# Performance work log

Hardware: AMD Instinct MI355X
Metric: run time of the kernel (lower is better)

The kernel has to match this reference:

```python
import jax, jax.numpy as jnp
import numpy as np

NUM_HEADS = 8
NUM_EXPERTS = 16384
NUM_KEYS = 128          # sqrt(NUM_EXPERTS)
TOPK = 16               # num_experts_per_head == product_key_topk
N_DIM = 1024
KEY_DIM = N_DIM // 2


def setup_inputs() -> dict:
    key = jax.random.key(0)
    k1, k2, k3, k4, k5 = jax.random.split(key, 5)
    x = jax.random.normal(k1, (1, 1024, N_DIM), dtype=jnp.float32)
    # torch Linear weight is (out_features, in_features)
    Wq = jax.random.normal(k2, (KEY_DIM * NUM_HEADS * 2, N_DIM), dtype=jnp.float32) * 0.02
    keys = jax.random.normal(k3, (NUM_HEADS, NUM_KEYS, 2, KEY_DIM), dtype=jnp.float32) * 0.02
    up_embed = jax.random.normal(k4, (NUM_EXPERTS * NUM_HEADS, N_DIM), dtype=jnp.float32)
    down_embed = jax.random.normal(k5, (NUM_EXPERTS * NUM_HEADS, N_DIM), dtype=jnp.float32)
    return {"x": x, "Wq": Wq, "keys": keys, "up_embed": up_embed, "down_embed": down_embed}


def reference(x, Wq, keys, up_embed, down_embed):
    b, n, d = x.shape
    # queries: Linear -> (b,n,2,h,kd) -> permute to (2,b,n,h,kd)
    q = (x @ Wq.T).reshape(b, n, 2, NUM_HEADS, KEY_DIM)
    q = jnp.transpose(q, (2, 0, 1, 3, 4))  # (p=2, b, n, h, kd)
    # sim: (p, b, n, h, num_keys)
    sim = jnp.einsum('pbnhd,hkpd->pbnhk', q, keys)
    scores_x, indices_x = jax.lax.top_k(sim[0], TOPK)  # (b,n,h,K)
    scores_y, indices_y = jax.lax.top_k(sim[1], TOPK)
    # cartesian product of the two top-k sets: (b,n,h,K*K)
    all_scores = (scores_x[..., :, None] + scores_y[..., None, :]).reshape(b, n, NUM_HEADS, TOPK * TOPK)
    all_indices = (indices_x[..., :, None] * NUM_KEYS + indices_y[..., None, :]).reshape(b, n, NUM_HEADS, TOPK * TOPK)
    scores, pk_indices = jax.lax.top_k(all_scores, TOPK)  # (b,n,h,K)
    indices = jnp.take_along_axis(all_indices, pk_indices, axis=-1)
    # separate embedding table per head
    head_offsets = jnp.arange(NUM_HEADS, dtype=indices.dtype) * NUM_EXPERTS
    indices = indices + head_offsets[None, None, :, None]
    weights_down = down_embed[indices]  # (b,n,h,K,d)
    weights_up = up_embed[indices]      # (b,n,h,K,d)
    h = jnp.einsum('bnd,bnhkd->bnhk', x, weights_down)
    h = jax.nn.gelu(h, approximate=False)
    h = jax.nn.softmax(scores, axis=-1) * h
    out = jnp.einsum('bnhk,bnhkd->bnd', h, weights_up)
    return out
```

## Files before the change

kernel.cpp:

```cpp
#include <hip/hip_runtime.h>
#include <math.h>


#define BK 16

__device__ __forceinline__ void mac16(double (&acc)[4][4], float4 av, float4 bv) {
  const double ax = av.x, ay = av.y, az = av.z, aw = av.w;
  const double bx = bv.x, by = bv.y, bz = bv.z, bw = bv.w;
  acc[0][0] += ax * bx; acc[0][1] += ax * by; acc[0][2] += ax * bz; acc[0][3] += ax * bw;
  acc[1][0] += ay * bx; acc[1][1] += ay * by; acc[1][2] += ay * bz; acc[1][3] += ay * bw;
  acc[2][0] += az * bx; acc[2][1] += az * by; acc[2][2] += az * bz; acc[2][3] += az * bw;
  acc[3][0] += aw * bx; acc[3][1] += aw * by; acc[3][2] += aw * bz; acc[3][3] += aw * bw;
}

__global__ __launch_bounds__(256) void fold_kernel(
    const float* __restrict__ keys, const float* __restrict__ Wq,
    float* __restrict__ M) {
  __shared__ float As[BK][68];
  __shared__ float Bs[BK][68];
  const int s = blockIdx.z, p = s >> 3, h = s & 7;
  const float* A = keys + h * 131072 + p * 512;
  const float* B = Wq + (p * 4096 + h * 512) * 1024;
  float* C = M + (p * 1024 + h * 128) * 1024;
  const int row0 = blockIdx.y * 64;
  const int d0 = blockIdx.x * 64;
  const int t = threadIdx.x;
  const int tx = t & 15, ty = t >> 4;
  const int arow = t >> 2, ac4 = (t & 3) * 4;
  const int brow = t >> 4, bd4 = (t & 15) * 4;
  double acc[4][4] = {};
  for (int k0 = 0; k0 < 512; k0 += BK) {
    float4 a4 = *(const float4*)(A + (row0 + arow) * 1024 + k0 + ac4);
    float4 b4 = *(const float4*)(B + (k0 + brow) * 1024 + d0 + bd4);
    As[ac4 + 0][arow] = a4.x; As[ac4 + 1][arow] = a4.y;
    As[ac4 + 2][arow] = a4.z; As[ac4 + 3][arow] = a4.w;
    *(float4*)&Bs[brow][bd4] = b4;
    __syncthreads();
#pragma unroll
    for (int kk = 0; kk < BK; ++kk) {
      float4 av = *(const float4*)&As[kk][ty * 4];
      float4 bv = *(const float4*)&Bs[kk][tx * 4];
      mac16(acc, av, bv);
    }
    __syncthreads();
  }
#pragma unroll
  for (int i = 0; i < 4; ++i) {
    float4 o = {(float)acc[i][0], (float)acc[i][1], (float)acc[i][2], (float)acc[i][3]};
    *(float4*)(C + (row0 + ty * 4 + i) * 1024 + d0 + tx * 4) = o;
  }
}

__global__ __launch_bounds__(256) void sim_kernel(
    const float* __restrict__ x, const float* __restrict__ M,
    float* __restrict__ sim) {
  __shared__ float As[BK][68];
  __shared__ float Bs[BK][68];
  const int n0 = blockIdx.y * 64;
  const int r0 = blockIdx.x * 64;
  const int t = threadIdx.x;
  const int tx = t & 15, ty = t >> 4;
  const int arow = t >> 2, ak4 = (t & 3) * 4;
  double acc[4][4] = {};
  for (int k0 = 0; k0 < 1024; k0 += BK) {
    float4 a4 = *(const float4*)(x + (n0 + arow) * 1024 + k0 + ak4);
    float4 b4 = *(const float4*)(M + (r0 + arow) * 1024 + k0 + ak4);
    As[ak4 + 0][arow] = a4.x; As[ak4 + 1][arow] = a4.y;
    As[ak4 + 2][arow] = a4.z; As[ak4 + 3][arow] = a4.w;
    Bs[ak4 + 0][arow] = b4.x; Bs[ak4 + 1][arow] = b4.y;
    Bs[ak4 + 2][arow] = b4.z; Bs[ak4 + 3][arow] = b4.w;
    __syncthreads();
#pragma unroll
    for (int kk = 0; kk < BK; ++kk) {
      float4 av = *(const float4*)&As[kk][ty * 4];
      float4 bv = *(const float4*)&Bs[kk][tx * 4];
      mac16(acc, av, bv);
    }
    __syncthreads();
  }
#pragma unroll
  for (int i = 0; i < 4; ++i) {
    float4 o = {(float)acc[i][0], (float)acc[i][1], (float)acc[i][2], (float)acc[i][3]};
    *(float4*)(sim + (n0 + ty * 4 + i) * 2048 + r0 + tx * 4) = o;
  }
}

__device__ __forceinline__ void insert16(float (&v)[16], int (&id)[16],
                                         float nv, int nid) {
  if (nv > v[15]) {
    v[15] = nv; id[15] = nid;
#pragma unroll
    for (int j = 15; j > 0; --j) {
      if (v[j] > v[j - 1]) {
        float tv = v[j]; v[j] = v[j - 1]; v[j - 1] = tv;
        int ti = id[j]; id[j] = id[j - 1]; id[j - 1] = ti;
      }
    }
  }
}

__global__ __launch_bounds__(256) void topk_kernel(
    const float* __restrict__ sim, int* __restrict__ rows,
    float* __restrict__ wts) {
  const int tid = blockIdx.x * 256 + threadIdx.x;
  const int n = tid >> 3, h = tid & 7;
  const float* sx = sim + n * 2048 + h * 128;
  const float* sy = sx + 1024;
  float vx[16], vy[16]; int ix[16], iy[16];
#pragma unroll
  for (int j = 0; j < 16; ++j) { vx[j] = -1e30f; vy[j] = -1e30f; ix[j] = 0; iy[j] = 0; }
  for (int k = 0; k < 128; ++k) {
    insert16(vx, ix, sx[k], k);
    insert16(vy, iy, sy[k], k);
  }
  constexpr int JMAX[16] = {16, 8, 5, 4, 3, 2, 2, 2, 1, 1, 1, 1, 1, 1, 1, 1};
  float cv[16]; int cid[16];
#pragma unroll
  for (int j = 0; j < 16; ++j) { cv[j] = -1e30f; cid[j] = 0; }
#pragma unroll
  for (int i = 0; i < 16; ++i) {
#pragma unroll
    for (int j = 0; j < 16; ++j) {
      if (j < JMAX[i]) {
        insert16(cv, cid, vx[i] + vy[j], ix[i] * 128 + iy[j]);
      }
    }
  }
  float e[16], se = 0.f;
#pragma unroll
  for (int j = 0; j < 16; ++j) { e[j] = expf(cv[j] - cv[0]); se += e[j]; }
  const float inv = 1.0f / se;
#pragma unroll
  for (int j = 0; j < 16; ++j) {
    rows[tid * 16 + j] = h * 16384 + cid[j];
    wts[tid * 16 + j] = e[j] * inv;
  }
}

__global__ __launch_bounds__(256) void gather_kernel(
    const float* __restrict__ x, const float* __restrict__ up,
    const float* __restrict__ down, const int* __restrict__ rows,
    const float* __restrict__ wts, float* __restrict__ out) {
  __shared__ float xs[1024];
  __shared__ float gs[128];
  __shared__ int rS[128];
  __shared__ float wS[128];
  const int n = blockIdx.x;
  const int t = threadIdx.x;
  ((float4*)xs)[t] = ((const float4*)(x + n * 1024))[t];
  if (t < 128) { rS[t] = rows[n * 128 + t]; wS[t] = wts[n * 128 + t]; }
  __syncthreads();
  const int wave = t >> 6, lane = t & 63;
  const float4* xp = (const float4*)xs;
  for (int it = 0; it < 32; ++it) {
    const int i = it * 4 + wave;
    const long row = rS[i];
    const float4* dp = (const float4*)(down + row * 1024);
    float acc = 0.f;
#pragma unroll
    for (int j = 0; j < 4; ++j) {
      float4 d4 = dp[lane + 64 * j];
      float4 x4 = xp[lane + 64 * j];
      acc += d4.x * x4.x + d4.y * x4.y + d4.z * x4.z + d4.w * x4.w;
    }
#pragma unroll
    for (int off = 32; off; off >>= 1) acc += __shfl_down(acc, off);
    if (lane == 0) {
      const float v = acc;
      const float g = 0.5f * v * (1.0f + erff(v * 0.70710678118654752f));
      gs[i] = g * wS[i];
    }
  }
  __syncthreads();
  float4 a = {0.f, 0.f, 0.f, 0.f};
  const float4* upb = (const float4*)up;
#pragma unroll 4
  for (int i = 0; i < 128; ++i) {
    const long row = rS[i];
    const float g = gs[i];
    float4 u = upb[row * 256 + t];
    a.x += g * u.x; a.y += g * u.y; a.z += g * u.z; a.w += g * u.w;
  }
  ((float4*)out)[n * 256 + t] = a;
}

extern "C" void kernel_launch(void* const* d_in, const int* in_sizes, int n_in,
                              void* d_out, int out_size, void* d_ws, size_t ws_size,
                              hipStream_t stream) {
  const float* x = (const float*)d_in[0];
  const float* Wq = (const float*)d_in[1];
  const float* keys = (const float*)d_in[2];
  const float* up = (const float*)d_in[3];
  const float* down = (const float*)d_in[4];
  float* out = (float*)d_out;
  float* ws = (float*)d_ws;
  float* M = ws;
  float* sim = ws + 2097152;
  int* rows = (int*)(ws + 4194304);
  float* wts = ws + 4325376;

  fold_kernel<<<dim3(16, 2, 16), 256, 0, stream>>>(keys, Wq, M);
  sim_kernel<<<dim3(32, 16, 1), 256, 0, stream>>>(x, M, sim);
  topk_kernel<<<32, 256, 0, stream>>>(sim, rows, wts);
  gather_kernel<<<1024, 256, 0, stream>>>(x, up, down, rows, wts, out);
}
```

Baseline: 1.316 ms.

## Store folded matrix in double, vectorize top-k loads, batch gather rows

```diff
diff --git a/kernel.cpp b/kernel.cpp
--- a/kernel.cpp
+++ b/kernel.cpp
@@ -4,24 +4,28 @@
 
 #define BK 16
 
-__device__ __forceinline__ void mac16(double (&acc)[4][4], float4 av, float4 bv) {
-  const double ax = av.x, ay = av.y, az = av.z, aw = av.w;
-  const double bx = bv.x, by = bv.y, bz = bv.z, bw = bv.w;
-  acc[0][0] += ax * bx; acc[0][1] += ax * by; acc[0][2] += ax * bz; acc[0][3] += ax * bw;
-  acc[1][0] += ay * bx; acc[1][1] += ay * by; acc[1][2] += ay * bz; acc[1][3] += ay * bw;
-  acc[2][0] += az * bx; acc[2][1] += az * by; acc[2][2] += az * bz; acc[2][3] += az * bw;
-  acc[3][0] += aw * bx; acc[3][1] += aw * by; acc[3][2] += aw * bz; acc[3][3] += aw * bw;
+__device__ __forceinline__ void mac16d(double (&acc)[4][4],
+    const double a0, const double a1, const double a2, const double a3,
+    const double b0, const double b1, const double b2, const double b3) {
+  acc[0][0] += a0 * b0; acc[0][1] += a0 * b1; acc[0][2] += a0 * b2; acc[0][3] += a0 * b3;
+  acc[1][0] += a1 * b0; acc[1][1] += a1 * b1; acc[1][2] += a1 * b2; acc[1][3] += a1 * b3;
+  acc[2][0] += a2 * b0; acc[2][1] += a2 * b1; acc[2][2] += a2 * b2; acc[2][3] += a2 * b3;
+  acc[3][0] += a3 * b0; acc[3][1] += a3 * b1; acc[3][2] += a3 * b2; acc[3][3] += a3 * b3;
+}
+
+__device__ __forceinline__ float dot4(const float4 a, const float4 b) {
+  return a.x * b.x + a.y * b.y + a.z * b.z + a.w * b.w;
 }
 
 __global__ __launch_bounds__(256) void fold_kernel(
     const float* __restrict__ keys, const float* __restrict__ Wq,
-    float* __restrict__ M) {
-  __shared__ float As[BK][68];
-  __shared__ float Bs[BK][68];
+    double* __restrict__ M) {
+  __shared__ double As[BK][68];
+  __shared__ double Bs[BK][68];
   const int s = blockIdx.z, p = s >> 3, h = s & 7;
   const float* A = keys + h * 131072 + p * 512;
   const float* B = Wq + (p * 4096 + h * 512) * 1024;
-  float* C = M + (p * 1024 + h * 128) * 1024;
+  double* C = M + (p * 1024 + h * 128) * 1024;
   const int row0 = blockIdx.y * 64;
   const int d0 = blockIdx.x * 64;
   const int t = threadIdx.x;
@@ -32,30 +36,34 @@
   for (int k0 = 0; k0 < 512; k0 += BK) {
     float4 a4 = *(const float4*)(A + (row0 + arow) * 1024 + k0 + ac4);
     float4 b4 = *(const float4*)(B + (k0 + brow) * 1024 + d0 + bd4);
-    As[ac4 + 0][arow] = a4.x; As[ac4 + 1][arow] = a4.y;
-    As[ac4 + 2][arow] = a4.z; As[ac4 + 3][arow] = a4.w;
-    *(float4*)&Bs[brow][bd4] = b4;
+    As[ac4 + 0][arow] = (double)a4.x; As[ac4 + 1][arow] = (double)a4.y;
+    As[ac4 + 2][arow] = (double)a4.z; As[ac4 + 3][arow] = (double)a4.w;
+    *(double2*)&Bs[brow][bd4 + 0] = make_double2((double)b4.x, (double)b4.y);
+    *(double2*)&Bs[brow][bd4 + 2] = make_double2((double)b4.z, (double)b4.w);
     __syncthreads();
 #pragma unroll
     for (int kk = 0; kk < BK; ++kk) {
-      float4 av = *(const float4*)&As[kk][ty * 4];
-      float4 bv = *(const float4*)&Bs[kk][tx * 4];
-      mac16(acc, av, bv);
+      const double2 a01 = *(const double2*)&As[kk][ty * 4];
+      const double2 a23 = *(const double2*)&As[kk][ty * 4 + 2];
+      const double2 b01 = *(const double2*)&Bs[kk][tx * 4];
+      const double2 b23 = *(const double2*)&Bs[kk][tx * 4 + 2];
+      mac16d(acc, a01.x, a01.y, a23.x, a23.y, b01.x, b01.y, b23.x, b23.y);
     }
     __syncthreads();
   }
 #pragma unroll
   for (int i = 0; i < 4; ++i) {
-    float4 o = {(float)acc[i][0], (float)acc[i][1], (float)acc[i][2], (float)acc[i][3]};
-    *(float4*)(C + (row0 + ty * 4 + i) * 1024 + d0 + tx * 4) = o;
+    double* cr = C + (row0 + ty * 4 + i) * 1024 + d0 + tx * 4;
+    *(double2*)(cr + 0) = make_double2(acc[i][0], acc[i][1]);
+    *(double2*)(cr + 2) = make_double2(acc[i][2], acc[i][3]);
   }
 }
 
 __global__ __launch_bounds__(256) void sim_kernel(
-    const float* __restrict__ x, const float* __restrict__ M,
+    const float* __restrict__ x, const double* __restrict__ M,
     float* __restrict__ sim) {
-  __shared__ float As[BK][68];
-  __shared__ float Bs[BK][68];
+  __shared__ double As[BK][68];
+  __shared__ double Bs[BK][68];
   const int n0 = blockIdx.y * 64;
   const int r0 = blockIdx.x * 64;
   const int t = threadIdx.x;
@@ -64,17 +72,21 @@
   double acc[4][4] = {};
   for (int k0 = 0; k0 < 1024; k0 += BK) {
     float4 a4 = *(const float4*)(x + (n0 + arow) * 1024 + k0 + ak4);
-    float4 b4 = *(const float4*)(M + (r0 + arow) * 1024 + k0 + ak4);
-    As[ak4 + 0][arow] = a4.x; As[ak4 + 1][arow] = a4.y;
-    As[ak4 + 2][arow] = a4.z; As[ak4 + 3][arow] = a4.w;
-    Bs[ak4 + 0][arow] = b4.x; Bs[ak4 + 1][arow] = b4.y;
-    Bs[ak4 + 2][arow] = b4.z; Bs[ak4 + 3][arow] = b4.w;
+    const double* mrow = M + (r0 + arow) * 1024 + k0 + ak4;
+    double2 b01 = *(const double2*)(mrow + 0);
+    double2 b23 = *(const double2*)(mrow + 2);
+    As[ak4 + 0][arow] = (double)a4.x; As[ak4 + 1][arow] = (double)a4.y;
+    As[ak4 + 2][arow] = (double)a4.z; As[ak4 + 3][arow] = (double)a4.w;
+    Bs[ak4 + 0][arow] = b01.x; Bs[ak4 + 1][arow] = b01.y;
+    Bs[ak4 + 2][arow] = b23.x; Bs[ak4 + 3][arow] = b23.y;
     __syncthreads();
 #pragma unroll
     for (int kk = 0; kk < BK; ++kk) {
-      float4 av = *(const float4*)&As[kk][ty * 4];
-      float4 bv = *(const float4*)&Bs[kk][tx * 4];
-      mac16(acc, av, bv);
+      const double2 a01 = *(const double2*)&As[kk][ty * 4];
+      const double2 a23 = *(const double2*)&As[kk][ty * 4 + 2];
+      const double2 b01v = *(const double2*)&Bs[kk][tx * 4];
+      const double2 b23v = *(const double2*)&Bs[kk][tx * 4 + 2];
+      mac16d(acc, a01.x, a01.y, a23.x, a23.y, b01v.x, b01v.y, b23v.x, b23v.y);
     }
     __syncthreads();
   }
@@ -104,14 +116,18 @@
     float* __restrict__ wts) {
   const int tid = blockIdx.x * 256 + threadIdx.x;
   const int n = tid >> 3, h = tid & 7;
-  const float* sx = sim + n * 2048 + h * 128;
-  const float* sy = sx + 1024;
+  const float4* sx4 = (const float4*)(sim + n * 2048 + h * 128);
+  const float4* sy4 = sx4 + 256;
   float vx[16], vy[16]; int ix[16], iy[16];
 #pragma unroll
   for (int j = 0; j < 16; ++j) { vx[j] = -1e30f; vy[j] = -1e30f; ix[j] = 0; iy[j] = 0; }
-  for (int k = 0; k < 128; ++k) {
-    insert16(vx, ix, sx[k], k);
-    insert16(vy, iy, sy[k], k);
+  for (int k = 0; k < 32; ++k) {
+    const float4 a = sx4[k];
+    const float4 b = sy4[k];
+    insert16(vx, ix, a.x, k * 4 + 0); insert16(vx, ix, a.y, k * 4 + 1);
+    insert16(vx, ix, a.z, k * 4 + 2); insert16(vx, ix, a.w, k * 4 + 3);
+    insert16(vy, iy, b.x, k * 4 + 0); insert16(vy, iy, b.y, k * 4 + 1);
+    insert16(vy, iy, b.z, k * 4 + 2); insert16(vy, iy, b.w, k * 4 + 3);
   }
   constexpr int JMAX[16] = {16, 8, 5, 4, 3, 2, 2, 2, 1, 1, 1, 1, 1, 1, 1, 1};
   float cv[16]; int cid[16];
@@ -152,29 +168,35 @@
   __syncthreads();
   const int wave = t >> 6, lane = t & 63;
   const float4* xp = (const float4*)xs;
-  for (int it = 0; it < 32; ++it) {
-    const int i = it * 4 + wave;
-    const long row = rS[i];
-    const float4* dp = (const float4*)(down + row * 1024);
-    float acc = 0.f;
-#pragma unroll
-    for (int j = 0; j < 4; ++j) {
-      float4 d4 = dp[lane + 64 * j];
-      float4 x4 = xp[lane + 64 * j];
-      acc += d4.x * x4.x + d4.y * x4.y + d4.z * x4.z + d4.w * x4.w;
-    }
-#pragma unroll
-    for (int off = 32; off; off >>= 1) acc += __shfl_down(acc, off);
+  const float4 xv0 = xp[lane], xv1 = xp[lane + 64];
+  const float4 xv2 = xp[lane + 128], xv3 = xp[lane + 192];
+  for (int it = 0; it < 16; ++it) {
+    const int i0 = it * 8 + wave * 2;
+    const long r0 = rS[i0], r1 = rS[i0 + 1];
+    const float4* dp0 = (const float4*)(down + r0 * 1024);
+    const float4* dp1 = (const float4*)(down + r1 * 1024);
+    const float4 d00 = dp0[lane], d01 = dp0[lane + 64];
+    const float4 d02 = dp0[lane + 128], d03 = dp0[lane + 192];
+    const float4 d10 = dp1[lane], d11 = dp1[lane + 64];
+    const float4 d12 = dp1[lane + 128], d13 = dp1[lane + 192];
+    float acc0 = dot4(d00, xv0) + dot4(d01, xv1) + dot4(d02, xv2) + dot4(d03, xv3);
+    float acc1 = dot4(d10, xv0) + dot4(d11, xv1) + dot4(d12, xv2) + dot4(d13, xv3);
+#pragma unroll
+    for (int off = 32; off; off >>= 1) {
+      acc0 += __shfl_down(acc0, off);
+      acc1 += __shfl_down(acc1, off);
+    }
     if (lane == 0) {
-      const float v = acc;
-      const float g = 0.5f * v * (1.0f + erff(v * 0.70710678118654752f));
-      gs[i] = g * wS[i];
+      const float g0 = 0.5f * acc0 * (1.0f + erff(acc0 * 0.70710678118654752f));
+      const float g1 = 0.5f * acc1 * (1.0f + erff(acc1 * 0.70710678118654752f));
+      gs[i0] = g0 * wS[i0];
+      gs[i0 + 1] = g1 * wS[i0 + 1];
     }
   }
   __syncthreads();
   float4 a = {0.f, 0.f, 0.f, 0.f};
   const float4* upb = (const float4*)up;
-#pragma unroll 4
+#pragma unroll 8
   for (int i = 0; i < 128; ++i) {
     const long row = rS[i];
     const float g = gs[i];
@@ -194,10 +216,10 @@
   const float* down = (const float*)d_in[4];
   float* out = (float*)d_out;
   float* ws = (float*)d_ws;
-  float* M = ws;
-  float* sim = ws + 2097152;
-  int* rows = (int*)(ws + 4194304);
-  float* wts = ws + 4325376;
+  double* M = (double*)ws;
+  float* sim = ws + 4194304;
+  int* rows = (int*)(ws + 6291456);
+  float* wts = ws + 6422528;
 
   fold_kernel<<<dim3(16, 2, 16), 256, 0, stream>>>(keys, Wq, M);
   sim_kernel<<<dim3(32, 16, 1), 256, 0, stream>>>(x, M, sim);
```

Result: slower. 1.351 ms (+2.6%).
